# Kernel tuning notes

Hardware: AMD Instinct MI355X
Metric: run time of the kernel (lower is better)

## Reference

```python
import jax, jax.numpy as jnp
import numpy as np

DIM = 1024
NUM_HEADS = 16
HEAD_DIM = DIM // NUM_HEADS
SCALE = HEAD_DIM ** -0.5


def setup_inputs() -> dict:
    key = jax.random.key(0)
    ks = jax.random.split(key, 6)
    B, N, C = 2, 2048, DIM
    std = 1.0 / np.sqrt(C)
    x = jax.random.normal(ks[0], (B, N, C), dtype=jnp.float32)
    wq = jax.random.normal(ks[1], (C, C), dtype=jnp.float32) * std
    wk = jax.random.normal(ks[2], (C, C), dtype=jnp.float32) * std
    wv = jax.random.normal(ks[3], (C, C), dtype=jnp.float32) * std
    w_proj = jax.random.normal(ks[4], (C, C), dtype=jnp.float32) * std
    b_proj = jax.random.normal(ks[5], (C,), dtype=jnp.float32) * 0.01
    return {"x": x, "wq": wq, "wk": wk, "wv": wv, "w_proj": w_proj, "b_proj": b_proj}


def reference(x, wq, wk, wv, w_proj, b_proj):
    B, N, C = x.shape
    H, D = NUM_HEADS, HEAD_DIM
    Nq = N // 2
    # q from first half of tokens; k, v from all tokens
    q = (x[:, :Nq] @ wq.T).reshape(B, Nq, H, D).transpose(0, 2, 1, 3)  # [B,H,Nq,D]
    k = (x @ wk.T).reshape(B, N, H, D).transpose(0, 2, 1, 3)           # [B,H,N,D]
    v = (x @ wv.T).reshape(B, N, H, D).transpose(0, 2, 1, 3)           # [B,H,N,D]
    attn = jnp.einsum('bhqd,bhkd->bhqk', q, k) * SCALE
    attn = jax.nn.softmax(attn, axis=-1)
    out = jnp.einsum('bhqk,bhkd->bhqd', attn, v)                       # [B,H,Nq,D]
    out = out.transpose(0, 2, 1, 3).reshape(B, Nq, C)
    return out @ w_proj.T + b_proj
```

## Files before the change

kernel.cpp:

```cpp
#include <hip/hip_runtime.h>

typedef _Float16 f16;
typedef _Float16 f16x8 __attribute__((ext_vector_type(8)));
typedef _Float16 f16x4 __attribute__((ext_vector_type(4)));
typedef float f32x4 __attribute__((ext_vector_type(4)));

#define MFMA_F16(a, b, c) __builtin_amdgcn_mfma_f32_16x16x32_f16(a, b, c, 0, 0, 0)

__device__ __forceinline__ void gld16(const void* g, void* l) {
  __builtin_amdgcn_global_load_lds(
      (const __attribute__((address_space(1))) unsigned int*)(unsigned long long)g,
      (__attribute__((address_space(3))) unsigned int*)(unsigned long long)l, 16, 0, 0);
}

__global__ __launch_bounds__(256) void cvt_x_kernel(const float* __restrict__ in,
                                                    f16* __restrict__ out, int n8) {
  int i = blockIdx.x * 256 + threadIdx.x;
  if (i >= n8) return;
  const float4* p = (const float4*)(in + (size_t)i * 8);
  float4 a = p[0], b = p[1];
  f16x8 o = {(f16)a.x, (f16)a.y, (f16)a.z, (f16)a.w,
             (f16)b.x, (f16)b.y, (f16)b.z, (f16)b.w};
  *(f16x8*)(out + (size_t)i * 8) = o;
}

__global__ __launch_bounds__(256) void cvt_w4_kernel(const float* __restrict__ w0,
                                                     const float* __restrict__ w1,
                                                     const float* __restrict__ w2,
                                                     const float* __restrict__ w3,
                                                     f16* __restrict__ out) {
  int i = blockIdx.x * 256 + threadIdx.x;
  int t = i >> 17, r = i & 131071;
  const float* w = (t == 0) ? w0 : (t == 1) ? w1 : (t == 2) ? w2 : w3;
  const float4* p = (const float4*)(w + (size_t)r * 8);
  float4 a = p[0], b = p[1];
  f16x8 o = {(f16)a.x, (f16)a.y, (f16)a.z, (f16)a.w,
             (f16)b.x, (f16)b.y, (f16)b.z, (f16)b.w};
  *(f16x8*)(out + (size_t)t * 1048576 + (size_t)r * 8) = o;
}

__global__ __launch_bounds__(256) void qkv_gemm_kernel(
    const f16* __restrict__ A, const f16* __restrict__ Wq,
    const f16* __restrict__ Wk, const f16* __restrict__ Wv,
    f16* __restrict__ Qo, f16* __restrict__ Ko, f16* __restrict__ VT) {
  __shared__ __align__(16) f16 As[2][128 * 64];
  __shared__ __align__(16) f16 Bs[2][128 * 64];
  const int bid = blockIdx.x + blockIdx.y * 8;
  const int swz = (bid & 7) * 80 + (bid >> 3);
  const int bx = swz & 7, y = swz >> 3;
  const f16* Bw;
  f16* Co = nullptr;
  int mt, isv = 0;
  if (y < 16) { Bw = Wq; Co = Qo; mt = (y & 7) | ((y >> 3) << 4); }
  else if (y < 48) { Bw = Wk; Co = Ko; mt = y - 16; }
  else { Bw = Wv; isv = 1; mt = y - 48; }
  const int m0 = mt * 128, n0 = bx * 128;
  const int tid = threadIdx.x, lane = tid & 63, w = tid >> 6;
  const int wr = w >> 1, wc = w & 1, g = lane >> 4, c = lane & 15;
  const int r_st = tid >> 3, t_st = tid & 7;

  auto stage = [&](int k0, int buf) {
#pragma unroll
    for (int i = 0; i < 4; ++i) {
      int row = r_st + i * 32;
      int sl = (t_st ^ (row & 7)) * 8;
      gld16(&A[(size_t)(m0 + row) * 1024 + k0 + sl], &As[buf][(row * 8 + t_st) * 8]);
      gld16(&Bw[(size_t)(n0 + row) * 1024 + k0 + sl], &Bs[buf][(row * 8 + t_st) * 8]);
    }
  };

  f32x4 acc[4][4] = {};

  stage(0, 0);
  __syncthreads();

  for (int t = 0; t < 16; ++t) {
    const int cur = t & 1;
    if (t < 15) stage((t + 1) * 64, cur ^ 1);
#pragma unroll
    for (int kb = 0; kb < 2; ++kb) {
      f16x8 af[4], bf[4];
#pragma unroll
      for (int m2 = 0; m2 < 4; ++m2)
        af[m2] = *(const f16x8*)&As[cur][(wr * 64 + m2 * 16 + c) * 64 +
                                         (((kb * 4 + g) ^ (c & 7)) * 8)];
#pragma unroll
      for (int nt = 0; nt < 4; ++nt)
        bf[nt] = *(const f16x8*)&Bs[cur][(wc * 64 + nt * 16 + c) * 64 +
                                         (((kb * 4 + g) ^ (c & 7)) * 8)];
#pragma unroll
      for (int m2 = 0; m2 < 4; ++m2)
#pragma unroll
        for (int nt = 0; nt < 4; ++nt)
          acc[m2][nt] = MFMA_F16(af[m2], bf[nt], acc[m2][nt]);
    }
    __syncthreads();
  }

  if (isv) {
    const int b = m0 >> 11;
    const int n_base = (m0 & 2047) + wr * 64 + g * 4;
#pragma unroll
    for (int m2 = 0; m2 < 4; ++m2)
#pragma unroll
      for (int nt = 0; nt < 4; ++nt) {
        int col = n0 + wc * 64 + nt * 16 + c;
        int h = col >> 6, d = col & 63;
        f16x4 pv = {(f16)acc[m2][nt][0], (f16)acc[m2][nt][1],
                    (f16)acc[m2][nt][2], (f16)acc[m2][nt][3]};
        *(f16x4*)&VT[((size_t)((b * 16 + h) * 64 + d)) * 2048 + n_base + m2 * 16] = pv;
      }
  } else {
#pragma unroll
    for (int m2 = 0; m2 < 4; ++m2)
#pragma unroll
      for (int nt = 0; nt < 4; ++nt) {
        int col = n0 + wc * 64 + nt * 16 + c;
#pragma unroll
        for (int r = 0; r < 4; ++r)
          Co[(size_t)(m0 + wr * 64 + m2 * 16 + g * 4 + r) * 1024 + col] =
              (f16)acc[m2][nt][r];
      }
  }
}

__global__ __launch_bounds__(256) void proj_gemm_kernel(
    const f16* __restrict__ A, const f16* __restrict__ Bw,
    float* __restrict__ C, const float* __restrict__ bias) {
  __shared__ __align__(16) f16 As[2][64 * 64];
  __shared__ __align__(16) f16 Bs[2][64 * 64];
  const int bid = blockIdx.x + blockIdx.y * 16;
  const int swz = (bid & 7) * 64 + (bid >> 3);
  const int m0 = (swz >> 4) * 64, n0 = (swz & 15) * 64;
  const int tid = threadIdx.x, lane = tid & 63, w = tid >> 6;
  const int wr = w >> 1, wc = w & 1, g = lane >> 4, c = lane & 15;
  const int r_st = tid >> 3, t_st = tid & 7;

  auto stage = [&](int k0, int buf) {
#pragma unroll
    for (int i = 0; i < 2; ++i) {
      int row = r_st + i * 32;
      int sl = (t_st ^ (row & 7)) * 8;
      gld16(&A[(size_t)(m0 + row) * 1024 + k0 + sl], &As[buf][(row * 8 + t_st) * 8]);
      gld16(&Bw[(size_t)(n0 + row) * 1024 + k0 + sl], &Bs[buf][(row * 8 + t_st) * 8]);
    }
  };

  f32x4 acc[2][2] = {};

  stage(0, 0);
  __syncthreads();

  for (int t = 0; t < 16; ++t) {
    const int cur = t & 1;
    if (t < 15) stage((t + 1) * 64, cur ^ 1);
#pragma unroll
    for (int kb = 0; kb < 2; ++kb) {
      f16x8 af[2], bf[2];
#pragma unroll
      for (int m2 = 0; m2 < 2; ++m2)
        af[m2] = *(const f16x8*)&As[cur][(wr * 32 + m2 * 16 + c) * 64 +
                                         (((kb * 4 + g) ^ (c & 7)) * 8)];
#pragma unroll
      for (int nt = 0; nt < 2; ++nt)
        bf[nt] = *(const f16x8*)&Bs[cur][(wc * 32 + nt * 16 + c) * 64 +
                                         (((kb * 4 + g) ^ (c & 7)) * 8)];
#pragma unroll
      for (int m2 = 0; m2 < 2; ++m2)
#pragma unroll
        for (int nt = 0; nt < 2; ++nt)
          acc[m2][nt] = MFMA_F16(af[m2], bf[nt], acc[m2][nt]);
    }
    __syncthreads();
  }

#pragma unroll
  for (int m2 = 0; m2 < 2; ++m2)
#pragma unroll
    for (int nt = 0; nt < 2; ++nt) {
      int col = n0 + wc * 32 + nt * 16 + c;
      float bv = bias[col];
#pragma unroll
      for (int r = 0; r < 4; ++r)
        C[(size_t)(m0 + wr * 32 + m2 * 16 + g * 4 + r) * 1024 + col] =
            acc[m2][nt][r] + bv;
    }
}

__global__ __launch_bounds__(256, 3) void attn_kernel(const f16* __restrict__ Q,
                                                      const f16* __restrict__ Kg,
                                                      const f16* __restrict__ VT,
                                                      f16* __restrict__ Opart,
                                                      float* __restrict__ ML) {
  __shared__ __align__(16) f16 Ks[2][64 * 64];
  __shared__ __align__(16) f16 Vs[64 * 64];
  __shared__ __align__(16) f16 Ps[4][32 * 64];
  const int flat = blockIdx.x;
  const int swz = (flat & 7) * 128 + (flat >> 3);
  const int qt = swz & 7, h = (swz >> 3) & 15;
  const int ch = (swz >> 7) & 3, b = swz >> 9;
  const int tid = threadIdx.x, lane = tid & 63, w = tid >> 6;
  const int g = lane >> 4, c = lane & 15;
  const int r_st = tid >> 3, t_st = tid & 7;

  const f16* Kbase = Kg + (size_t)(b * 2048 + ch * 512) * 1024 + h * 64;
  const f16* Vbase = VT + ((size_t)((b * 16 + h) * 64)) * 2048 + ch * 512;

  f16x8 qf[2][2];
#pragma unroll
  for (int qs = 0; qs < 2; ++qs) {
    const f16* qp =
        Q + (size_t)(b * 2048 + qt * 128 + w * 32 + qs * 16 + c) * 1024 + h * 64;
    qf[qs][0] = *(const f16x8*)(qp + g * 8);
    qf[qs][1] = *(const f16x8*)(qp + 32 + g * 8);
#pragma unroll
    for (int j = 0; j < 8; ++j) {
      qf[qs][0][j] = (f16)((float)qf[qs][0][j] * 0.1803368801f);
      qf[qs][1][j] = (f16)((float)qf[qs][1][j] * 0.1803368801f);
    }
  }

  auto stageK = [&](int t, int buf) {
#pragma unroll
    for (int i = 0; i < 2; ++i) {
      int row = r_st + i * 32;
      int sl = (t_st ^ (row & 7)) * 8;
      gld16(&Kbase[(size_t)(t * 64 + row) * 1024 + sl],
            &Ks[buf][(row * 8 + t_st) * 8]);
    }
  };
  auto stageV = [&](int t) {
#pragma unroll
    for (int i = 0; i < 2; ++i) {
      int row = r_st + i * 32;
      int sl = (t_st ^ (row & 7)) * 8;
      gld16(&Vbase[(size_t)row * 2048 + t * 64 + sl], &Vs[(row * 8 + t_st) * 8]);
    }
  };

  f32x4 oaccT[4][2] = {};
  float l_part[2] = {0.f, 0.f};

  stageK(0, 0);
  stageV(0);
  asm volatile("s_waitcnt vmcnt(0)" ::: "memory");
  __builtin_amdgcn_s_barrier();
  __builtin_amdgcn_sched_barrier(0);

  for (int t = 0; t < 8; ++t) {
    const int cur = t & 1;
    if (t < 7) stageK(t + 1, cur ^ 1);

#pragma unroll
    for (int qs = 0; qs < 2; ++qs) {
      f32x4 s[4] = {};
#pragma unroll
      for (int kt = 0; kt < 4; ++kt) {
        f16x8 kf0 =
            *(const f16x8*)&Ks[cur][(kt * 16 + c) * 64 + ((g ^ (c & 7)) * 8)];
        f16x8 kf1 =
            *(const f16x8*)&Ks[cur][(kt * 16 + c) * 64 + (((4 + g) ^ (c & 7)) * 8)];
        s[kt] = MFMA_F16(kf0, qf[qs][0], s[kt]);
        s[kt] = MFMA_F16(kf1, qf[qs][1], s[kt]);
      }
      float rs = 0.f;
#pragma unroll
      for (int kt = 0; kt < 4; ++kt)
#pragma unroll
        for (int r = 0; r < 4; ++r) {
          float p = exp2f(s[kt][r]);
          s[kt][r] = p;
          rs += p;
        }
      l_part[qs] += rs;
#pragma unroll
      for (int kt = 0; kt < 4; ++kt) {
        f16x4 pv = {(f16)s[kt][0], (f16)s[kt][1], (f16)s[kt][2], (f16)s[kt][3]};
        *(f16x4*)&Ps[w][(qs * 16 + c) * 64 +
                        (((kt * 2 + (g >> 1)) ^ (c & 7)) * 8) + (g & 1) * 4] = pv;
      }
    }

    if (t < 7) {
      asm volatile("s_waitcnt vmcnt(2)" ::: "memory");
    } else {
      asm volatile("s_waitcnt vmcnt(0)" ::: "memory");
    }
    __builtin_amdgcn_s_barrier();
    __builtin_amdgcn_sched_barrier(0);

#pragma unroll
    for (int kb = 0; kb < 2; ++kb) {
      f16x8 pf0 =
          *(const f16x8*)&Ps[w][c * 64 + (((kb * 4 + g) ^ (c & 7)) * 8)];
      f16x8 pf1 =
          *(const f16x8*)&Ps[w][(16 + c) * 64 + (((kb * 4 + g) ^ (c & 7)) * 8)];
#pragma unroll
      for (int dt = 0; dt < 4; ++dt) {
        f16x8 vf = *(const f16x8*)&Vs[(dt * 16 + c) * 64 +
                                      (((kb * 4 + g) ^ (c & 7)) * 8)];
        oaccT[dt][0] = MFMA_F16(vf, pf0, oaccT[dt][0]);
        oaccT[dt][1] = MFMA_F16(vf, pf1, oaccT[dt][1]);
      }
    }

    asm volatile("s_waitcnt vmcnt(0)" ::: "memory");
    __builtin_amdgcn_s_barrier();
    __builtin_amdgcn_sched_barrier(0);
    if (t < 7) stageV(t + 1);
  }

  float lf[2];
#pragma unroll
  for (int qs = 0; qs < 2; ++qs) {
    float l = l_part[qs];
    l += __shfl_xor(l, 16);
    l += __shfl_xor(l, 32);
    lf[qs] = l;
  }
#pragma unroll
  for (int qs = 0; qs < 2; ++qs) {
    float li = 1.f / lf[qs];
#pragma unroll
    for (int dt = 0; dt < 4; ++dt) {
      f16x4 ov = {(f16)(oaccT[dt][qs][0] * li), (f16)(oaccT[dt][qs][1] * li),
                  (f16)(oaccT[dt][qs][2] * li), (f16)(oaccT[dt][qs][3] * li)};
      *(f16x4*)&Opart[(size_t)ch * 2097152 +
                      (size_t)(b * 1024 + qt * 128 + w * 32 + qs * 16 + c) * 1024 +
                      h * 64 + dt * 16 + g * 4] = ov;
    }
  }
  if (lane < 16) {
#pragma unroll
    for (int qs = 0; qs < 2; ++qs)
      ML[ch * 32768 + (b * 1024 + qt * 128 + w * 32 + qs * 16 + lane) * 16 + h] =
          lf[qs];
  }
}

__global__ __launch_bounds__(256) void combine_kernel(const f16* __restrict__ Opart,
                                                      const float* __restrict__ ML,
                                                      f16* __restrict__ O16) {
  int i = blockIdx.x * 256 + threadIdx.x;
  int row = i >> 7;
  int h = (i & 127) >> 3;
  float l0 = ML[row * 16 + h];
  float l1 = ML[32768 + row * 16 + h];
  float l2 = ML[65536 + row * 16 + h];
  float l3 = ML[98304 + row * 16 + h];
  float inv = 1.f / (l0 + l1 + l2 + l3);
  f16x8 o0 = *(const f16x8*)&Opart[(size_t)i * 8];
  f16x8 o1 = *(const f16x8*)&Opart[2097152 + (size_t)i * 8];
  f16x8 o2 = *(const f16x8*)&Opart[4194304 + (size_t)i * 8];
  f16x8 o3 = *(const f16x8*)&Opart[6291456 + (size_t)i * 8];
  f16x8 r;
#pragma unroll
  for (int j = 0; j < 8; ++j)
    r[j] = (f16)((l0 * (float)o0[j] + l1 * (float)o1[j] + l2 * (float)o2[j] +
                  l3 * (float)o3[j]) * inv);
  *(f16x8*)&O16[(size_t)i * 8] = r;
}

extern "C" void kernel_launch(void* const* d_in, const int* in_sizes, int n_in,
                              void* d_out, int out_size, void* d_ws, size_t ws_size,
                              hipStream_t stream) {
  const float* x = (const float*)d_in[0];
  const float* wq = (const float*)d_in[1];
  const float* wk = (const float*)d_in[2];
  const float* wv = (const float*)d_in[3];
  const float* wp = (const float*)d_in[4];
  const float* bp = (const float*)d_in[5];
  float* out = (float*)d_out;

  char* p = (char*)d_ws;
  f16* x16 = (f16*)p;   p += (size_t)4194304 * 2;
  f16* w16 = (f16*)p;   p += (size_t)4 * 1048576 * 2;
  f16* Q16 = (f16*)p;   p += (size_t)4194304 * 2;
  f16* K16 = (f16*)p;   p += (size_t)4194304 * 2;
  f16* VT16 = (f16*)p;  p += (size_t)4194304 * 2;
  f16* Opart = (f16*)p; p += (size_t)8388608 * 2;
  f16* O16 = (f16*)p;   p += (size_t)2097152 * 2;

  f16* wq16 = w16;
  f16* wk16 = w16 + 1048576;
  f16* wv16 = w16 + 2 * 1048576;
  f16* wp16 = w16 + 3 * 1048576;

  cvt_x_kernel<<<4194304 / 8 / 256, 256, 0, stream>>>(x, x16, 4194304 / 8);
  cvt_w4_kernel<<<4 * 131072 / 256, 256, 0, stream>>>(wq, wk, wv, wp, w16);

  qkv_gemm_kernel<<<dim3(8, 80), 256, 0, stream>>>(x16, wq16, wk16, wv16, Q16, K16,
                                                   VT16);

  float* MLp = (float*)x16;
  attn_kernel<<<dim3(1024), 256, 0, stream>>>(Q16, K16, VT16, Opart, MLp);
  combine_kernel<<<1024, 256, 0, stream>>>(Opart, MLp, O16);

  proj_gemm_kernel<<<dim3(16, 32), 256, 0, stream>>>(O16, wp16, out, bp);
}
```

Measured before the change: 95.89 us.

## Rewrite attention kernel with 32x32 MFMA, register-resident K/V and in-register P

Replaces the LDS-staged attention with a version where each wave loads its K and V fragments straight from global memory into registers and uses 32x32x16 MFMAs. The softmax probabilities are packed to f16 and exchanged across lanes with shuffles instead of going through shared memory. The key dimension is split between wave pairs, whose partial outputs are reduced through LDS at the end. The grid doubles to 2048 blocks of 64 query rows each. This removes the per-tile barriers and LDS traffic, at the cost of redundant global loads of K/V per wave and an extra reduction step.

```diff
diff --git a/kernel.cpp b/kernel.cpp
--- a/kernel.cpp
+++ b/kernel.cpp
@@ -4,14 +4,22 @@
 typedef _Float16 f16x8 __attribute__((ext_vector_type(8)));
 typedef _Float16 f16x4 __attribute__((ext_vector_type(4)));
 typedef float f32x4 __attribute__((ext_vector_type(4)));
+typedef float f32x16 __attribute__((ext_vector_type(16)));
 
 #define MFMA_F16(a, b, c) __builtin_amdgcn_mfma_f32_16x16x32_f16(a, b, c, 0, 0, 0)
+#define MFMA32(a, b, c) __builtin_amdgcn_mfma_f32_32x32x16_f16(a, b, c, 0, 0, 0)
 
 __device__ __forceinline__ void gld16(const void* g, void* l) {
   __builtin_amdgcn_global_load_lds(
       (const __attribute__((address_space(1))) unsigned int*)(unsigned long long)g,
       (__attribute__((address_space(3))) unsigned int*)(unsigned long long)l, 16, 0, 0);
 }
+
+__device__ __forceinline__ int pkrtz(float a, float b) {
+  return __builtin_bit_cast(int, __builtin_amdgcn_cvt_pkrtz(a, b));
+}
+
+union U8 { int i[4]; f16x8 v; };
 
 __global__ __launch_bounds__(256) void cvt_x_kernel(const float* __restrict__ in,
                                                     f16* __restrict__ out, int n8) {
@@ -187,154 +195,131 @@
     }
 }
 
-__global__ __launch_bounds__(256, 3) void attn_kernel(const f16* __restrict__ Q,
-                                                      const f16* __restrict__ Kg,
-                                                      const f16* __restrict__ VT,
-                                                      f16* __restrict__ Opart,
-                                                      float* __restrict__ ML) {
-  __shared__ __align__(16) f16 Ks[2][64 * 64];
-  __shared__ __align__(16) f16 Vs[64 * 64];
-  __shared__ __align__(16) f16 Ps[4][32 * 64];
+__global__ __launch_bounds__(256) void attn_kernel(const f16* __restrict__ Q,
+                                                   const f16* __restrict__ Kg,
+                                                   const f16* __restrict__ VT,
+                                                   f16* __restrict__ Opart,
+                                                   float* __restrict__ ML) {
+  __shared__ float Ored[2][64][32];
+  __shared__ float Lred[2][2][32];
+  __shared__ f16 Otr[2][32][70];
   const int flat = blockIdx.x;
-  const int swz = (flat & 7) * 128 + (flat >> 3);
-  const int qt = swz & 7, h = (swz >> 3) & 15;
-  const int ch = (swz >> 7) & 3, b = swz >> 9;
+  const int swz = (flat & 7) * 256 + (flat >> 3);
+  const int qt = swz & 15, h = (swz >> 4) & 15;
+  const int ch = (swz >> 8) & 3, b = swz >> 10;
   const int tid = threadIdx.x, lane = tid & 63, w = tid >> 6;
-  const int g = lane >> 4, c = lane & 15;
-  const int r_st = tid >> 3, t_st = tid & 7;
-
-  const f16* Kbase = Kg + (size_t)(b * 2048 + ch * 512) * 1024 + h * 64;
-  const f16* Vbase = VT + ((size_t)((b * 16 + h) * 64)) * 2048 + ch * 512;
-
-  f16x8 qf[2][2];
-#pragma unroll
-  for (int qs = 0; qs < 2; ++qs) {
-    const f16* qp =
-        Q + (size_t)(b * 2048 + qt * 128 + w * 32 + qs * 16 + c) * 1024 + h * 64;
-    qf[qs][0] = *(const f16x8*)(qp + g * 8);
-    qf[qs][1] = *(const f16x8*)(qp + 32 + g * 8);
-#pragma unroll
-    for (int j = 0; j < 8; ++j) {
-      qf[qs][0][j] = (f16)((float)qf[qs][0][j] * 0.1803368801f);
-      qf[qs][1][j] = (f16)((float)qf[qs][1][j] * 0.1803368801f);
-    }
-  }
-
-  auto stageK = [&](int t, int buf) {
-#pragma unroll
-    for (int i = 0; i < 2; ++i) {
-      int row = r_st + i * 32;
-      int sl = (t_st ^ (row & 7)) * 8;
-      gld16(&Kbase[(size_t)(t * 64 + row) * 1024 + sl],
-            &Ks[buf][(row * 8 + t_st) * 8]);
-    }
+  const int kh = w & 1, qh = w >> 1;
+  const int l31 = lane & 31, h5 = lane >> 5;
+  const bool lo = lane < 32;
+
+  const f16* Kp =
+      Kg + (size_t)(b * 2048 + ch * 512 + kh * 32 + l31) * 1024 + h * 64 + h5 * 8;
+  const f16* Vp = VT + ((size_t)((b * 16 + h) * 64 + l31)) * 2048 + ch * 512 +
+                  kh * 32 + h5 * 8;
+  const f16* Qp =
+      Q + (size_t)(b * 2048 + qt * 64 + qh * 32 + l31) * 1024 + h * 64 + h5 * 8;
+
+  f16x8 qf[4];
+#pragma unroll
+  for (int ks = 0; ks < 4; ++ks) {
+    qf[ks] = *(const f16x8*)(Qp + ks * 16);
+#pragma unroll
+    for (int j = 0; j < 8; ++j)
+      qf[ks][j] = (f16)((float)qf[ks][j] * 0.1803368801f);
+  }
+
+  f16x8 kc0, kc1, kc2, kc3, vc0, vc1, vc2, vc3;
+  auto loadK = [&](int t) {
+    const f16* p = Kp + (size_t)t * 65536;
+    kc0 = *(const f16x8*)(p);
+    kc1 = *(const f16x8*)(p + 16);
+    kc2 = *(const f16x8*)(p + 32);
+    kc3 = *(const f16x8*)(p + 48);
   };
-  auto stageV = [&](int t) {
-#pragma unroll
-    for (int i = 0; i < 2; ++i) {
-      int row = r_st + i * 32;
-      int sl = (t_st ^ (row & 7)) * 8;
-      gld16(&Vbase[(size_t)row * 2048 + t * 64 + sl], &Vs[(row * 8 + t_st) * 8]);
-    }
+  auto loadV = [&](int t) {
+    const f16* p = Vp + t * 64;
+    vc0 = *(const f16x8*)(p);
+    vc1 = *(const f16x8*)(p + 16);
+    vc2 = *(const f16x8*)(p + 65536);
+    vc3 = *(const f16x8*)(p + 65536 + 16);
   };
 
-  f32x4 oaccT[4][2] = {};
-  float l_part[2] = {0.f, 0.f};
-
-  stageK(0, 0);
-  stageV(0);
-  asm volatile("s_waitcnt vmcnt(0)" ::: "memory");
-  __builtin_amdgcn_s_barrier();
-  __builtin_amdgcn_sched_barrier(0);
+  f32x16 o0 = {}, o1 = {};
+  float lp = 0.f;
+
+  loadK(0);
+  loadV(0);
 
   for (int t = 0; t < 8; ++t) {
-    const int cur = t & 1;
-    if (t < 7) stageK(t + 1, cur ^ 1);
-
-#pragma unroll
-    for (int qs = 0; qs < 2; ++qs) {
-      f32x4 s[4] = {};
-#pragma unroll
-      for (int kt = 0; kt < 4; ++kt) {
-        f16x8 kf0 =
-            *(const f16x8*)&Ks[cur][(kt * 16 + c) * 64 + ((g ^ (c & 7)) * 8)];
-        f16x8 kf1 =
-            *(const f16x8*)&Ks[cur][(kt * 16 + c) * 64 + (((4 + g) ^ (c & 7)) * 8)];
-        s[kt] = MFMA_F16(kf0, qf[qs][0], s[kt]);
-        s[kt] = MFMA_F16(kf1, qf[qs][1], s[kt]);
-      }
-      float rs = 0.f;
-#pragma unroll
-      for (int kt = 0; kt < 4; ++kt)
-#pragma unroll
-        for (int r = 0; r < 4; ++r) {
-          float p = exp2f(s[kt][r]);
-          s[kt][r] = p;
-          rs += p;
-        }
-      l_part[qs] += rs;
-#pragma unroll
-      for (int kt = 0; kt < 4; ++kt) {
-        f16x4 pv = {(f16)s[kt][0], (f16)s[kt][1], (f16)s[kt][2], (f16)s[kt][3]};
-        *(f16x4*)&Ps[w][(qs * 16 + c) * 64 +
-                        (((kt * 2 + (g >> 1)) ^ (c & 7)) * 8) + (g & 1) * 4] = pv;
-      }
-    }
-
-    if (t < 7) {
-      asm volatile("s_waitcnt vmcnt(2)" ::: "memory");
-    } else {
-      asm volatile("s_waitcnt vmcnt(0)" ::: "memory");
-    }
-    __builtin_amdgcn_s_barrier();
-    __builtin_amdgcn_sched_barrier(0);
-
-#pragma unroll
-    for (int kb = 0; kb < 2; ++kb) {
-      f16x8 pf0 =
-          *(const f16x8*)&Ps[w][c * 64 + (((kb * 4 + g) ^ (c & 7)) * 8)];
-      f16x8 pf1 =
-          *(const f16x8*)&Ps[w][(16 + c) * 64 + (((kb * 4 + g) ^ (c & 7)) * 8)];
-#pragma unroll
-      for (int dt = 0; dt < 4; ++dt) {
-        f16x8 vf = *(const f16x8*)&Vs[(dt * 16 + c) * 64 +
-                                      (((kb * 4 + g) ^ (c & 7)) * 8)];
-        oaccT[dt][0] = MFMA_F16(vf, pf0, oaccT[dt][0]);
-        oaccT[dt][1] = MFMA_F16(vf, pf1, oaccT[dt][1]);
-      }
-    }
-
-    asm volatile("s_waitcnt vmcnt(0)" ::: "memory");
-    __builtin_amdgcn_s_barrier();
-    __builtin_amdgcn_sched_barrier(0);
-    if (t < 7) stageV(t + 1);
-  }
-
-  float lf[2];
-#pragma unroll
-  for (int qs = 0; qs < 2; ++qs) {
-    float l = l_part[qs];
-    l += __shfl_xor(l, 16);
-    l += __shfl_xor(l, 32);
-    lf[qs] = l;
-  }
-#pragma unroll
-  for (int qs = 0; qs < 2; ++qs) {
-    float li = 1.f / lf[qs];
-#pragma unroll
-    for (int dt = 0; dt < 4; ++dt) {
-      f16x4 ov = {(f16)(oaccT[dt][qs][0] * li), (f16)(oaccT[dt][qs][1] * li),
-                  (f16)(oaccT[dt][qs][2] * li), (f16)(oaccT[dt][qs][3] * li)};
-      *(f16x4*)&Opart[(size_t)ch * 2097152 +
-                      (size_t)(b * 1024 + qt * 128 + w * 32 + qs * 16 + c) * 1024 +
-                      h * 64 + dt * 16 + g * 4] = ov;
-    }
-  }
-  if (lane < 16) {
-#pragma unroll
-    for (int qs = 0; qs < 2; ++qs)
-      ML[ch * 32768 + (b * 1024 + qt * 128 + w * 32 + qs * 16 + lane) * 16 + h] =
-          lf[qs];
+    f32x16 s = {};
+    s = MFMA32(kc0, qf[0], s);
+    s = MFMA32(kc1, qf[1], s);
+    s = MFMA32(kc2, qf[2], s);
+    s = MFMA32(kc3, qf[3], s);
+    if (t < 7) loadK(t + 1);
+
+    float e[16];
+#pragma unroll
+    for (int i = 0; i < 16; ++i) {
+      e[i] = exp2f(s[i]);
+      lp += e[i];
+    }
+    int c01 = pkrtz(e[0], e[1]), c23 = pkrtz(e[2], e[3]);
+    int c45 = pkrtz(e[4], e[5]), c67 = pkrtz(e[6], e[7]);
+    int d01 = pkrtz(e[8], e[9]), d23 = pkrtz(e[10], e[11]);
+    int d45 = pkrtz(e[12], e[13]), d67 = pkrtz(e[14], e[15]);
+    int xc01 = __shfl_xor(c01, 32), xc23 = __shfl_xor(c23, 32);
+    int xc45 = __shfl_xor(c45, 32), xc67 = __shfl_xor(c67, 32);
+    int xd01 = __shfl_xor(d01, 32), xd23 = __shfl_xor(d23, 32);
+    int xd45 = __shfl_xor(d45, 32), xd67 = __shfl_xor(d67, 32);
+    U8 pb0, pb1;
+    pb0.i[0] = lo ? c01 : xc45;
+    pb0.i[1] = lo ? c23 : xc67;
+    pb0.i[2] = lo ? xc01 : c45;
+    pb0.i[3] = lo ? xc23 : c67;
+    pb1.i[0] = lo ? d01 : xd45;
+    pb1.i[1] = lo ? d23 : xd67;
+    pb1.i[2] = lo ? xd01 : d45;
+    pb1.i[3] = lo ? xd23 : d67;
+
+    o0 = MFMA32(vc0, pb0.v, o0);
+    o0 = MFMA32(vc1, pb1.v, o0);
+    o1 = MFMA32(vc2, pb0.v, o1);
+    o1 = MFMA32(vc3, pb1.v, o1);
+    if (t < 7) loadV(t + 1);
+  }
+
+  float l_own = lp + __shfl_xor(lp, 32);
+  if (kh == 1) {
+#pragma unroll
+    for (int reg = 0; reg < 16; ++reg) {
+      int row = (reg & 3) + 8 * (reg >> 2) + 4 * h5;
+      Ored[qh][row][l31] = o0[reg];
+      Ored[qh][32 + row][l31] = o1[reg];
+    }
+    if (lo) Lred[qh][1][l31] = l_own;
+  } else {
+    if (lo) Lred[qh][0][l31] = l_own;
+  }
+  __syncthreads();
+  if (kh == 0) {
+    float lt = Lred[qh][0][l31] + Lred[qh][1][l31];
+    float li = 1.f / lt;
+#pragma unroll
+    for (int reg = 0; reg < 16; ++reg) {
+      int row = (reg & 3) + 8 * (reg >> 2) + 4 * h5;
+      Otr[qh][l31][row] = (f16)((o0[reg] + Ored[qh][row][l31]) * li);
+      Otr[qh][l31][32 + row] = (f16)((o1[reg] + Ored[qh][32 + row][l31]) * li);
+    }
+#pragma unroll
+    for (int rep = 0; rep < 4; ++rep) {
+      f16x8 ov = *(const f16x8*)&Otr[qh][lane >> 1][(lane & 1) * 32 + rep * 8];
+      *(f16x8*)&Opart[(size_t)ch * 2097152 +
+                      (size_t)(b * 1024 + qt * 64 + qh * 32 + (lane >> 1)) * 1024 +
+                      h * 64 + (lane & 1) * 32 + rep * 8] = ov;
+    }
+    if (lo)
+      ML[ch * 32768 + (b * 1024 + qt * 64 + qh * 32 + l31) * 16 + h] = lt;
   }
 }
 
@@ -393,7 +378,7 @@
                                                    VT16);
 
   float* MLp = (float*)x16;
-  attn_kernel<<<dim3(1024), 256, 0, stream>>>(Q16, K16, VT16, Opart, MLp);
+  attn_kernel<<<dim3(2048), 256, 0, stream>>>(Q16, K16, VT16, Opart, MLp);
   combine_kernel<<<1024, 256, 0, stream>>>(Opart, MLp, O16);
 
   proj_gemm_kernel<<<dim3(16, 32), 256, 0, stream>>>(O16, wp16, out, bp);
```

After: 127.9 us. +33.4%, slower.
